# Optimization experiments

Hardware: AMD Instinct MI355X
Metric: run time of the kernel (lower is better)

## Reference

```python
import jax, jax.numpy as jnp
import numpy as np

PMASK_SLOPE = 5.0
SAMPLE_SLOPE = 10.0
SPARSITY = 0.125
MAX_ITERS = 1000
ATOL = 1e-3

B, H, W = 64, 256, 256


def _rejection_sample(x, key):
    """Regenerate uniform noise until mean(x > prob) ~= mean(x), like
    ThresholdRandomMaskSigmoidV1.forward. Returns (result, prob)."""
    tgt = jnp.mean(x)

    def draw(k):
        k, sub = jax.random.split(k)
        prob = jax.random.uniform(sub, x.shape, x.dtype)
        result = (x > prob).astype(x.dtype)
        return k, prob, result

    def cond(state):
        _, _, result, count = state
        ok = jnp.isclose(jnp.mean(result), tgt, atol=ATOL)
        return jnp.logical_and(jnp.logical_not(ok), count <= MAX_ITERS)

    def body(state):
        k, _, _, count = state
        k, prob, result = draw(k)
        return (k, prob, result, count + 1)

    k, prob0, result0 = draw(key)
    _, prob, result, _ = jax.lax.while_loop(cond, body, (k, prob0, result0, jnp.int32(0)))
    return result, prob


def _make_threshold(key):
    @jax.custom_vjp
    def thresh(x):
        return _rejection_sample(x, key)[0]

    def fwd(x):
        result, prob = _rejection_sample(x, key)
        return result, (x, prob)

    def bwd(res, g):
        x, prob = res
        e = jnp.exp(-SAMPLE_SLOPE * (x - prob))
        return (SAMPLE_SLOPE * e / (e + 1.0) ** 2 * g,)

    thresh.defvjp(fwd, bwd)
    return thresh

_thresh = _make_threshold(jax.random.key(42))


def setup_inputs() -> dict:
    key = jax.random.key(0)
    kx, kw = jax.random.split(key)
    x = jax.random.normal(kx, (B, 1, H, W), dtype=jnp.float32)
    eps = 1e-4
    u = jax.random.uniform(kw, (1, 1, H, W), dtype=jnp.float32, minval=eps, maxval=1.0 - eps)
    weight = -jnp.log(1.0 / u - 1.0) / PMASK_SLOPE  # ProbMask.reset_parameters
    return {"x": x, "weight": weight}


def reference(x, weight):
    # ProbMask: broadcast weight against x[..., 0:1] then sigmoid(slope * .)
    prob1 = jax.nn.sigmoid(PMASK_SLOPE * (0.0 * x[..., 0:1] + weight))  # [B,1,H,W]

    # RescaleProbMap
    xbar = jnp.mean(prob1)
    r = SPARSITY / xbar
    beta = (1.0 - SPARSITY) / (1.0 - xbar)
    le = (r < 1.0).astype(prob1.dtype)
    prob2 = le * prob1 * r + (1.0 - le) * (1.0 - (1.0 - prob1) * beta)

    # ThresholdRandomMaskSigmoidV1 (rejection-sampled binary mask)
    mask = _thresh(prob2)  # [B,1,H,W]

    # FFT: torch.rfft(x, 2, onesided=False) -> full 2D FFT of real input
    fc = jnp.fft.fft2(x[:, 0])                       # [B,H,W] complex
    fft = jnp.stack([fc.real, fc.imag], axis=1)      # [B,2,H,W]

    # UnderSample: multiply both channels by the mask
    u_k = fft * mask                                  # broadcast [B,1,H,W]

    # iFFT over spatial dims
    uc = u_k[:, 0] + 1j * u_k[:, 1]
    ic = jnp.fft.ifft2(uc)
    uifft = jnp.stack([ic.real, ic.imag], axis=1)    # [B,2,H,W]

    # ComplexAbs
    complex_abs = jnp.sqrt(uifft[:, 0:1] ** 2 + uifft[:, 1:2] ** 2)

    return (uifft, complex_abs, mask, fft, u_k)
```

## Files before the change

kernel.cpp:

```cpp
#include <hip/hip_runtime.h>


#define HW_N   65536

__device__ __forceinline__ float f_add(float a, float b){ float d; asm("v_add_f32 %0, %1, %2" : "=v"(d) : "v"(a), "v"(b)); return d; }
__device__ __forceinline__ float f_sub(float a, float b){ float d; asm("v_sub_f32 %0, %1, %2" : "=v"(d) : "v"(a), "v"(b)); return d; }
__device__ __forceinline__ float f_mul(float a, float b){ float d; asm("v_mul_f32 %0, %1, %2" : "=v"(d) : "v"(a), "v"(b)); return d; }
__device__ __forceinline__ float f_fma(float a, float b, float c){ return __builtin_fmaf(a, b, c); }

__device__ float xla_expf(float x0) {
  float x = fminf(x0, 88.723f);
  float m = floorf(f_fma(x, 1.44269504088896341f, 0.5f));
  float r = f_fma(m, -0.693359375f, x);
  r = f_fma(m, 2.12194440e-4f, r);
  float r2 = f_mul(r, r);
  float r3 = f_mul(r2, r);
  float y  = f_fma(1.9875691500E-4f, r, 1.3981999507E-3f);
  float y1 = f_fma(4.1665795894E-2f, r, 1.6666665459E-1f);
  float y2 = f_add(r, 1.0f);
  y  = f_fma(y, r, 8.3334519073E-3f);
  y1 = f_fma(y1, r, 5.0000001201E-1f);
  y  = f_fma(y, r3, y1);
  y  = f_fma(y, r2, y2);
  float p2n = __uint_as_float((unsigned)(((int)m + 127) << 23));
  float res = f_mul(y, p2n);
  if (x0 < -104.0f) res = 0.0f;
  return fmaxf(res, x0);
}

__device__ __forceinline__ float xla_sigmoid(float q) {
  float e = xla_expf(-q);
  return 1.0f / f_add(1.0f, e);
}

__host__ __device__ __forceinline__ void tf2x32(unsigned k0, unsigned k1,
                                                unsigned c0, unsigned c1,
                                                unsigned& o0, unsigned& o1) {
  unsigned ks2 = k0 ^ k1 ^ 0x1BD11BDAu;
  unsigned x0 = c0 + k0, x1 = c1 + k1;
#define TF_R(r) { x0 += x1; x1 = (x1 << r) | (x1 >> (32 - r)); x1 ^= x0; }
  TF_R(13) TF_R(15) TF_R(26) TF_R(6)
  x0 += k1;  x1 += ks2 + 1u;
  TF_R(17) TF_R(29) TF_R(16) TF_R(24)
  x0 += ks2; x1 += k0 + 2u;
  TF_R(13) TF_R(15) TF_R(26) TF_R(6)
  x0 += k0;  x1 += k1 + 3u;
  TF_R(17) TF_R(29) TF_R(16) TF_R(24)
  x0 += k1;  x1 += ks2 + 4u;
  TF_R(13) TF_R(15) TF_R(26) TF_R(6)
  x0 += ks2; x1 += k0 + 5u;
#undef TF_R
  o0 = x0; o1 = x1;
}

__global__ void k_prep(const float* __restrict__ weight, float* __restrict__ ws) {
  int i = blockIdx.x * 256 + threadIdx.x;
  if (i < HW_N) {
    float q = f_mul(5.0f, weight[i]);
    ws[i] = xla_sigmoid(q);
  }
  if (blockIdx.x == 0 && threadIdx.x < 128) {
    double ang = -2.0 * 3.14159265358979323846 * (double)threadIdx.x / 256.0;
    float* tw = ws + 2 * HW_N;
    tw[2 * threadIdx.x]     = (float)cos(ang);
    tw[2 * threadIdx.x + 1] = (float)sin(ang);
  }
}

__global__ void k_xbar(float* __restrict__ ws) {
  __shared__ float lanes[32];
  int l = threadIdx.x;
  if (l < 32) {
    float acc = 0.0f;
    for (int k = 0; k < 2048; ++k)
      acc = f_add(acc, ws[32 * k + l]);
    lanes[l] = acc;
  }
  __syncthreads();
  if (l == 0) {
    float A[32];
    for (int i = 0; i < 32; ++i) A[i] = lanes[i];
    float c[16];
    for (int k = 0; k < 16; ++k) c[k] = f_add(A[k], A[k + 16]);
    float d[8];
    for (int k = 0; k < 8; ++k)  d[k] = f_add(c[k], c[k + 8]);
    float e[4];
    for (int k = 0; k < 4; ++k)  e[k] = f_add(d[k], d[k + 4]);
    float f2[2];
    for (int k = 0; k < 2; ++k)  f2[k] = f_add(e[k], e[k + 2]);
    float S = f_add(f2[0], f2[1]);
    float xbar = S / 65536.0f;
    float r    = 0.125f / xbar;
    float le   = (r < 1.0f) ? 1.0f : 0.0f;
    float beta = 0.875f / f_sub(1.0f, xbar);
    float* sc = ws + 2 * HW_N + 256;
    sc[0] = r; sc[1] = le; sc[2] = beta;
  }
}

__global__ void k_prob2(float* __restrict__ ws) {
  int i = blockIdx.x * 256 + threadIdx.x;
  if (i >= HW_N) return;
  const float* sc = ws + 2 * HW_N + 256;
  float r = sc[0], le = sc[1], beta = sc[2];
  float p = ws[i];
  float t1 = f_mul(f_mul(le, p), r);
  float t2 = f_mul(f_sub(1.0f, le),
                   f_sub(1.0f, f_mul(f_sub(1.0f, p), beta)));
  ws[HW_N + i] = f_add(t1, t2);
}

__global__ void k_mask(const float* __restrict__ ws, float* __restrict__ mask,
                       unsigned sk0, unsigned sk1) {
  unsigned i = blockIdx.x * 256u + threadIdx.x;
  unsigned o0, o1;
  tf2x32(sk0, sk1, 0u, i, o0, o1);
  unsigned bits = o0 ^ o1;
  float f = __uint_as_float((bits >> 9) | 0x3f800000u) - 1.0f;
  float p2 = ws[HW_N + (i & 65535u)];
  mask[i] = (p2 > f) ? 1.0f : 0.0f;
}

__device__ __forceinline__ int brev8(int i) { return (int)(__brev((unsigned)i) >> 24); }

__device__ __forceinline__ void fft256(float* re, float* im, int k,
                                       const float* __restrict__ tw, float sgn) {
  for (int s = 1; s <= 8; ++s) {
    __syncthreads();
    int hm = 1 << (s - 1);
    int j  = k & (hm - 1);
    int i1 = ((k >> (s - 1)) << s) + j;
    int i2 = i1 + hm;
    int ti = j << (8 - s);
    float wr = tw[2 * ti], wi = sgn * tw[2 * ti + 1];
    float vr = re[i2], vi = im[i2];
    float tr  = vr * wr - vi * wi;
    float tii = vr * wi + vi * wr;
    float ur = re[i1], ui = im[i1];
    re[i1] = ur + tr;  im[i1] = ui + tii;
    re[i2] = ur - tr;  im[i2] = ui - tii;
  }
  __syncthreads();
}

__global__ void k_fft_row(const float* __restrict__ x, float* __restrict__ fft,
                          const float* __restrict__ ws) {
  __shared__ float re[2][256], im[2][256];
  const float* tw = ws + 2 * HW_N;
  int line = blockIdx.x * 2 + (threadIdx.x >> 7);
  int k = threadIdx.x & 127, r = threadIdx.x >> 7;
  int b = line >> 8, h = line & 255;
  const float* src = x + b * 65536 + h * 256;
  re[r][k]       = src[brev8(k)];        im[r][k]       = 0.0f;
  re[r][k + 128] = src[brev8(k + 128)];  im[r][k + 128] = 0.0f;
  fft256(re[r], im[r], k, tw, 1.0f);
  float* dre = fft + b * 131072 + h * 256;
  float* dim = dre + 65536;
  dre[k]       = re[r][k];        dim[k]       = im[r][k];
  dre[k + 128] = re[r][k + 128];  dim[k + 128] = im[r][k + 128];
}

__global__ __launch_bounds__(256) void k_colpass(float* __restrict__ fftbuf,
                                                 const float* __restrict__ mask,
                                                 float* __restrict__ uk,
                                                 float* __restrict__ vbuf,
                                                 const float* __restrict__ ws) {
  __shared__ float lre[256][32];
  __shared__ float lim[256][32];
  const float* tw = ws + 2 * HW_N;
  int bid = blockIdx.x;
  int b = bid >> 3, c0 = (bid & 7) << 5;
  int t = threadIdx.x;
  int cl = t & 31, rg = t >> 5;
  float* pre = fftbuf + b * 131072;
  float* pim = pre + 65536;

  for (int it = 0; it < 32; ++it) {
    int r = (it << 3) + rg;
    int cc = (cl + r) & 31;
    lre[r][cc] = pre[r * 256 + c0 + cl];
    lim[r][cc] = pim[r * 256 + c0 + cl];
  }
  __syncthreads();

  for (int hm = 128, sh = 7; hm >= 1; hm >>= 1, --sh) {
    for (int kk = 0; kk < 16; ++kk) {
      int k = (kk << 3) + rg;
      int j = k & (hm - 1);
      int i1 = ((k >> sh) << (sh + 1)) + j;
      int i2 = i1 + hm;
      int ti = j << (7 - sh);
      float wr = tw[2 * ti], wi = tw[2 * ti + 1];
      int cc1 = (cl + i1) & 31, cc2 = (cl + i2) & 31;
      float ur = lre[i1][cc1], ui = lim[i1][cc1];
      float vr = lre[i2][cc2], vi = lim[i2][cc2];
      float dr = ur - vr, di = ui - vi;
      lre[i1][cc1] = ur + vr;            lim[i1][cc1] = ui + vi;
      lre[i2][cc2] = dr * wr - di * wi;  lim[i2][cc2] = dr * wi + di * wr;
    }
    __syncthreads();
  }

  const float* mk = mask + b * 65536;
  float* ukre = uk + b * 131072;
  float* ukim = ukre + 65536;
  for (int it = 0; it < 32; ++it) {
    int p = (it << 3) + rg;
    int f = brev8(p);
    int cc = (cl + p) & 31;
    float vr = lre[p][cc], vi = lim[p][cc];
    int gi = f * 256 + c0 + cl;
    pre[gi] = vr;  pim[gi] = vi;
    float m = mk[gi];
    float mvr = vr * m, mvi = vi * m;
    ukre[gi] = mvr;  ukim[gi] = mvi;
    lre[p][cc] = mvr;  lim[p][cc] = mvi;
  }
  __syncthreads();

  for (int s = 1; s <= 8; ++s) {
    int hm = 1 << (s - 1);
    for (int kk = 0; kk < 16; ++kk) {
      int k = (kk << 3) + rg;
      int j = k & (hm - 1);
      int i1 = ((k >> (s - 1)) << s) + j;
      int i2 = i1 + hm;
      int ti = j << (8 - s);
      float wr = tw[2 * ti], wi = -tw[2 * ti + 1];
      int cc1 = (cl + i1) & 31, cc2 = (cl + i2) & 31;
      float vr = lre[i2][cc2], vi = lim[i2][cc2];
      float tr = vr * wr - vi * wi, tii = vr * wi + vi * wr;
      float ur = lre[i1][cc1], ui = lim[i1][cc1];
      lre[i1][cc1] = ur + tr;  lim[i1][cc1] = ui + tii;
      lre[i2][cc2] = ur - tr;  lim[i2][cc2] = ui - tii;
    }
    __syncthreads();
  }

  float* vre = vbuf + b * 131072;
  float* vim = vre + 65536;
  for (int it = 0; it < 32; ++it) {
    int r = (it << 3) + rg;
    int cc = (cl + r) & 31;
    vre[r * 256 + c0 + cl] = lre[r][cc];
    vim[r * 256 + c0 + cl] = lim[r][cc];
  }
}

__global__ void k_irow(float* __restrict__ uif, float* __restrict__ cabs,
                       const float* __restrict__ ws) {
  __shared__ float re[2][256], im[2][256];
  const float* tw = ws + 2 * HW_N;
  int line = blockIdx.x * 2 + (threadIdx.x >> 7);
  int k = threadIdx.x & 127, r = threadIdx.x >> 7;
  int b = line >> 8, h = line & 255;
  float* sre = uif + b * 131072 + h * 256;
  float* sim = sre + 65536;
  re[r][k]       = sre[brev8(k)];        im[r][k]       = sim[brev8(k)];
  re[r][k + 128] = sre[brev8(k + 128)];  im[r][k + 128] = sim[brev8(k + 128)];
  fft256(re[r], im[r], k, tw, -1.0f);
  const float scale = 1.0f / 65536.0f;
  float* ab = cabs + b * 65536 + h * 256;
  for (int t2 = 0; t2 < 2; ++t2) {
    int i = k + t2 * 128;
    float vr = re[r][i] * scale, vi = im[r][i] * scale;
    sre[i] = vr;  sim[i] = vi;
    ab[i] = sqrtf(vr * vr + vi * vi);
  }
}

extern "C" void kernel_launch(void* const* d_in, const int* in_sizes, int n_in,
                              void* d_out, int out_size, void* d_ws, size_t ws_size,
                              hipStream_t stream) {
  const float* x      = (const float*)d_in[0];
  const float* weight = (const float*)d_in[1];
  float* out = (float*)d_out;
  float* ws  = (float*)d_ws;

  float* uifft = out;
  float* cabs  = out + 8388608;
  float* mask  = out + 12582912;
  float* fft   = out + 16777216;
  float* uk    = out + 25165824;

  unsigned sk0, sk1;
  tf2x32(0u, 42u, 0u, 1u, sk0, sk1);

  k_prep   <<<256, 256, 0, stream>>>(weight, ws);
  k_xbar   <<<1, 64, 0, stream>>>(ws);
  k_prob2  <<<256, 256, 0, stream>>>(ws);
  k_mask   <<<16384, 256, 0, stream>>>(ws, mask, sk0, sk1);
  k_fft_row<<<8192, 256, 0, stream>>>(x, fft, ws);
  k_colpass<<<512, 256, 0, stream>>>(fft, mask, uk, uifft, ws);
  k_irow   <<<8192, 256, 0, stream>>>(uifft, cabs, ws);
}
```

Baseline: 279.3 us.

## Switch row and column FFTs to radix-4 and fuse prob2 into mask

Replaces the radix-2 FFTs (8 stages) in the row, column and inverse-row kernels with radix-4 butterflies (4 stages). This halves the shared-memory passes and barriers, and the row kernels now process 4 lines per block with padded LDS to avoid bank conflicts. Twiddle tables grow to 256 entries for the 3*ti indices, and bit reversal becomes base-4 digit reversal. The prob2 rescale is folded into the mask kernel, removing one launch and a global round trip. Floating-point rounding may differ slightly from the radix-2 ordering.

New measurement: 274.5 us. About the same (-1.7%).

```diff
diff --git a/kernel.cpp b/kernel.cpp
--- a/kernel.cpp
+++ b/kernel.cpp
@@ -1,7 +1,8 @@
 #include <hip/hip_runtime.h>
 
 
-#define HW_N   65536
+#define HW_N 65536
+#define LMAP(a) ((a) + ((a) >> 5))
 
 __device__ __forceinline__ float f_add(float a, float b){ float d; asm("v_add_f32 %0, %1, %2" : "=v"(d) : "v"(a), "v"(b)); return d; }
 __device__ __forceinline__ float f_sub(float a, float b){ float d; asm("v_sub_f32 %0, %1, %2" : "=v"(d) : "v"(a), "v"(b)); return d; }
@@ -27,7 +28,6 @@
   if (x0 < -104.0f) res = 0.0f;
   return fmaxf(res, x0);
 }
-
 __device__ __forceinline__ float xla_sigmoid(float q) {
   float e = xla_expf(-q);
   return 1.0f / f_add(1.0f, e);
@@ -53,17 +53,27 @@
   o0 = x0; o1 = x1;
 }
 
+__device__ __forceinline__ int rev4(int p) {
+  return ((p & 3) << 6) | (((p >> 2) & 3) << 4) | (((p >> 4) & 3) << 2) | ((p >> 6) & 3);
+}
+
+#define CMULW(xr, xi, ti) { float wr = tw[2*(ti)], wi = tw[2*(ti)+1]; \
+  float nr = xr*wr - xi*wi; xi = xr*wi + xi*wr; xr = nr; }
+#define CMULWC(xr, xi, ti) { float wr = tw[2*(ti)], wi = tw[2*(ti)+1]; \
+  float nr = xr*wr + xi*wi; xi = xi*wr - xr*wi; xr = nr; }
+
 __global__ void k_prep(const float* __restrict__ weight, float* __restrict__ ws) {
   int i = blockIdx.x * 256 + threadIdx.x;
   if (i < HW_N) {
     float q = f_mul(5.0f, weight[i]);
     ws[i] = xla_sigmoid(q);
   }
-  if (blockIdx.x == 0 && threadIdx.x < 128) {
-    double ang = -2.0 * 3.14159265358979323846 * (double)threadIdx.x / 256.0;
-    float* tw = ws + 2 * HW_N;
-    tw[2 * threadIdx.x]     = (float)cos(ang);
-    tw[2 * threadIdx.x + 1] = (float)sin(ang);
+  if (blockIdx.x == 0) {
+    int t = threadIdx.x;
+    double ang = -2.0 * 3.14159265358979323846 * (double)t / 256.0;
+    float* tw = ws + 131072;
+    tw[2 * t]     = (float)cos(ang);
+    tw[2 * t + 1] = (float)sin(ang);
   }
 }
 
@@ -93,71 +103,77 @@
     float r    = 0.125f / xbar;
     float le   = (r < 1.0f) ? 1.0f : 0.0f;
     float beta = 0.875f / f_sub(1.0f, xbar);
-    float* sc = ws + 2 * HW_N + 256;
+    float* sc = ws + 131584;
     sc[0] = r; sc[1] = le; sc[2] = beta;
   }
-}
-
-__global__ void k_prob2(float* __restrict__ ws) {
-  int i = blockIdx.x * 256 + threadIdx.x;
-  if (i >= HW_N) return;
-  const float* sc = ws + 2 * HW_N + 256;
-  float r = sc[0], le = sc[1], beta = sc[2];
-  float p = ws[i];
-  float t1 = f_mul(f_mul(le, p), r);
-  float t2 = f_mul(f_sub(1.0f, le),
-                   f_sub(1.0f, f_mul(f_sub(1.0f, p), beta)));
-  ws[HW_N + i] = f_add(t1, t2);
 }
 
 __global__ void k_mask(const float* __restrict__ ws, float* __restrict__ mask,
                        unsigned sk0, unsigned sk1) {
   unsigned i = blockIdx.x * 256u + threadIdx.x;
+  const float* sc = ws + 131584;
+  float r = sc[0], le = sc[1], beta = sc[2];
+  float p1 = ws[i & 65535u];
+  float t1 = f_mul(f_mul(le, p1), r);
+  float t2 = f_mul(f_sub(1.0f, le),
+                   f_sub(1.0f, f_mul(f_sub(1.0f, p1), beta)));
+  float p2 = f_add(t1, t2);
   unsigned o0, o1;
   tf2x32(sk0, sk1, 0u, i, o0, o1);
   unsigned bits = o0 ^ o1;
   float f = __uint_as_float((bits >> 9) | 0x3f800000u) - 1.0f;
-  float p2 = ws[HW_N + (i & 65535u)];
   mask[i] = (p2 > f) ? 1.0f : 0.0f;
 }
 
-__device__ __forceinline__ int brev8(int i) { return (int)(__brev((unsigned)i) >> 24); }
-
-__device__ __forceinline__ void fft256(float* re, float* im, int k,
-                                       const float* __restrict__ tw, float sgn) {
-  for (int s = 1; s <= 8; ++s) {
-    __syncthreads();
-    int hm = 1 << (s - 1);
-    int j  = k & (hm - 1);
-    int i1 = ((k >> (s - 1)) << s) + j;
-    int i2 = i1 + hm;
-    int ti = j << (8 - s);
-    float wr = tw[2 * ti], wi = sgn * tw[2 * ti + 1];
-    float vr = re[i2], vi = im[i2];
-    float tr  = vr * wr - vi * wi;
-    float tii = vr * wi + vi * wr;
-    float ur = re[i1], ui = im[i1];
-    re[i1] = ur + tr;  im[i1] = ui + tii;
-    re[i2] = ur - tr;  im[i2] = ui - tii;
-  }
-  __syncthreads();
-}
-
-__global__ void k_fft_row(const float* __restrict__ x, float* __restrict__ fft,
-                          const float* __restrict__ ws) {
-  __shared__ float re[2][256], im[2][256];
-  const float* tw = ws + 2 * HW_N;
-  int line = blockIdx.x * 2 + (threadIdx.x >> 7);
-  int k = threadIdx.x & 127, r = threadIdx.x >> 7;
+__global__ __launch_bounds__(256) void k_fft_row(const float* __restrict__ x,
+                                                 float* __restrict__ fftb,
+                                                 const float* __restrict__ ws) {
+  __shared__ float re[4][264], im[4][264];
+  const float* tw = ws + 131072;
+  int rl = threadIdx.x >> 6, bf = threadIdx.x & 63;
+  int line = blockIdx.x * 4 + rl;
   int b = line >> 8, h = line & 255;
   const float* src = x + b * 65536 + h * 256;
-  re[r][k]       = src[brev8(k)];        im[r][k]       = 0.0f;
-  re[r][k + 128] = src[brev8(k + 128)];  im[r][k + 128] = 0.0f;
-  fft256(re[r], im[r], k, tw, 1.0f);
-  float* dre = fft + b * 131072 + h * 256;
+  float* lre = re[rl];
+  float* lim = im[rl];
+  #pragma unroll
+  for (int t2 = 0; t2 < 4; ++t2) {
+    int p = t2 * 64 + bf;
+    lre[LMAP(p)] = src[rev4(p)];
+    lim[LMAP(p)] = 0.0f;
+  }
+  #pragma unroll
+  for (int s2 = 0; s2 < 4; ++s2) {
+    __syncthreads();
+    int lq = 2 * s2, qq = 1 << lq;
+    int j = bf & (qq - 1), g = bf >> lq;
+    int base = (g << (lq + 2)) + j;
+    int u = 64 >> lq;
+    int a0 = base, a1 = base + qq, a2 = base + 2 * qq, a3 = base + 3 * qq;
+    float s0r = lre[LMAP(a0)], s0i = lim[LMAP(a0)];
+    float s1r = lre[LMAP(a1)], s1i = lim[LMAP(a1)];
+    float s2r = lre[LMAP(a2)], s2i = lim[LMAP(a2)];
+    float s3r = lre[LMAP(a3)], s3i = lim[LMAP(a3)];
+    int ti = j * u;
+    CMULW(s1r, s1i, ti); CMULW(s2r, s2i, 2 * ti); CMULW(s3r, s3i, 3 * ti);
+    float p0r = s0r + s2r, p0i = s0i + s2i;
+    float m0r = s0r - s2r, m0i = s0i - s2i;
+    float p1r = s1r + s3r, p1i = s1i + s3i;
+    float m1r = s1r - s3r, m1i = s1i - s3i;
+    lre[LMAP(a0)] = p0r + p1r;  lim[LMAP(a0)] = p0i + p1i;
+    lre[LMAP(a1)] = m0r + m1i;  lim[LMAP(a1)] = m0i - m1r;
+    lre[LMAP(a2)] = p0r - p1r;  lim[LMAP(a2)] = p0i - p1i;
+    lre[LMAP(a3)] = m0r - m1i;  lim[LMAP(a3)] = m0i + m1r;
+  }
+  __syncthreads();
+  float* dre = fftb + b * 131072 + h * 256;
   float* dim = dre + 65536;
-  dre[k]       = re[r][k];        dim[k]       = im[r][k];
-  dre[k + 128] = re[r][k + 128];  dim[k + 128] = im[r][k + 128];
+  #pragma unroll
+  for (int t2 = 0; t2 < 4; ++t2) {
+    int p = t2 * 64 + bf;
+    dre[p] = lre[LMAP(p)];
+    dim[p] = lim[LMAP(p)];
+  }
 }
 
 __global__ __launch_bounds__(256) void k_colpass(float* __restrict__ fftbuf,
@@ -167,7 +183,7 @@
                                                  const float* __restrict__ ws) {
   __shared__ float lre[256][32];
   __shared__ float lim[256][32];
-  const float* tw = ws + 2 * HW_N;
+  const float* tw = ws + 131072;
   int bid = blockIdx.x;
   int b = bid >> 3, c0 = (bid & 7) << 5;
   int t = threadIdx.x;
@@ -181,32 +197,46 @@
     lre[r][cc] = pre[r * 256 + c0 + cl];
     lim[r][cc] = pim[r * 256 + c0 + cl];
   }
-  __syncthreads();
-
-  for (int hm = 128, sh = 7; hm >= 1; hm >>= 1, --sh) {
-    for (int kk = 0; kk < 16; ++kk) {
-      int k = (kk << 3) + rg;
-      int j = k & (hm - 1);
-      int i1 = ((k >> sh) << (sh + 1)) + j;
-      int i2 = i1 + hm;
-      int ti = j << (7 - sh);
-      float wr = tw[2 * ti], wi = tw[2 * ti + 1];
-      int cc1 = (cl + i1) & 31, cc2 = (cl + i2) & 31;
-      float ur = lre[i1][cc1], ui = lim[i1][cc1];
-      float vr = lre[i2][cc2], vi = lim[i2][cc2];
-      float dr = ur - vr, di = ui - vi;
-      lre[i1][cc1] = ur + vr;            lim[i1][cc1] = ui + vi;
-      lre[i2][cc2] = dr * wr - di * wi;  lim[i2][cc2] = dr * wi + di * wr;
+
+  #pragma unroll
+  for (int s2 = 0; s2 < 4; ++s2) {
+    __syncthreads();
+    int lq = 6 - 2 * s2, qq = 1 << lq;
+    int u = 1 << (2 * s2);
+    for (int kk = 0; kk < 8; ++kk) {
+      int bf = (kk << 3) + rg;
+      int j = bf & (qq - 1), g = bf >> lq;
+      int base = (g << (lq + 2)) + j;
+      int a0 = base, a1 = base + qq, a2 = base + 2 * qq, a3 = base + 3 * qq;
+      int c_0 = (cl + a0) & 31, c_1 = (cl + a1) & 31,
+          c_2 = (cl + a2) & 31, c_3 = (cl + a3) & 31;
+      float ar = lre[a0][c_0], ai = lim[a0][c_0];
+      float br = lre[a1][c_1], bi = lim[a1][c_1];
+      float cr = lre[a2][c_2], ci = lim[a2][c_2];
+      float dr = lre[a3][c_3], di = lim[a3][c_3];
+      float apcr = ar + cr, apci = ai + ci;
+      float amcr = ar - cr, amci = ai - ci;
+      float bpdr = br + dr, bpdi = bi + di;
+      float bmdr = br - dr, bmdi = bi - di;
+      int ti = j * u;
+      float y1r = amcr + bmdi, y1i = amci - bmdr;
+      float y2r = apcr - bpdr, y2i = apci - bpdi;
+      float y3r = amcr - bmdi, y3i = amci + bmdr;
+      CMULW(y1r, y1i, ti); CMULW(y2r, y2i, 2 * ti); CMULW(y3r, y3i, 3 * ti);
+      lre[a0][c_0] = apcr + bpdr;  lim[a0][c_0] = apci + bpdi;
+      lre[a1][c_1] = y1r;          lim[a1][c_1] = y1i;
+      lre[a2][c_2] = y2r;          lim[a2][c_2] = y2i;
+      lre[a3][c_3] = y3r;          lim[a3][c_3] = y3i;
     }
-    __syncthreads();
-  }
+  }
+  __syncthreads();
 
   const float* mk = mask + b * 65536;
   float* ukre = uk + b * 131072;
   float* ukim = ukre + 65536;
   for (int it = 0; it < 32; ++it) {
     int p = (it << 3) + rg;
-    int f = brev8(p);
+    int f = rev4(p);
     int cc = (cl + p) & 31;
     float vr = lre[p][cc], vi = lim[p][cc];
     int gi = f * 256 + c0 + cl;
@@ -216,26 +246,36 @@
     ukre[gi] = mvr;  ukim[gi] = mvi;
     lre[p][cc] = mvr;  lim[p][cc] = mvi;
   }
-  __syncthreads();
-
-  for (int s = 1; s <= 8; ++s) {
-    int hm = 1 << (s - 1);
-    for (int kk = 0; kk < 16; ++kk) {
-      int k = (kk << 3) + rg;
-      int j = k & (hm - 1);
-      int i1 = ((k >> (s - 1)) << s) + j;
-      int i2 = i1 + hm;
-      int ti = j << (8 - s);
-      float wr = tw[2 * ti], wi = -tw[2 * ti + 1];
-      int cc1 = (cl + i1) & 31, cc2 = (cl + i2) & 31;
-      float vr = lre[i2][cc2], vi = lim[i2][cc2];
-      float tr = vr * wr - vi * wi, tii = vr * wi + vi * wr;
-      float ur = lre[i1][cc1], ui = lim[i1][cc1];
-      lre[i1][cc1] = ur + tr;  lim[i1][cc1] = ui + tii;
-      lre[i2][cc2] = ur - tr;  lim[i2][cc2] = ui - tii;
+
+  #pragma unroll
+  for (int s2 = 0; s2 < 4; ++s2) {
+    __syncthreads();
+    int lq = 2 * s2, qq = 1 << lq;
+    int u = 64 >> lq;
+    for (int kk = 0; kk < 8; ++kk) {
+      int bf = (kk << 3) + rg;
+      int j = bf & (qq - 1), g = bf >> lq;
+      int base = (g << (lq + 2)) + j;
+      int a0 = base, a1 = base + qq, a2 = base + 2 * qq, a3 = base + 3 * qq;
+      int c_0 = (cl + a0) & 31, c_1 = (cl + a1) & 31,
+          c_2 = (cl + a2) & 31, c_3 = (cl + a3) & 31;
+      float s0r = lre[a0][c_0], s0i = lim[a0][c_0];
+      float s1r = lre[a1][c_1], s1i = lim[a1][c_1];
+      float s2r = lre[a2][c_2], s2i = lim[a2][c_2];
+      float s3r = lre[a3][c_3], s3i = lim[a3][c_3];
+      int ti = j * u;
+      CMULWC(s1r, s1i, ti); CMULWC(s2r, s2i, 2 * ti); CMULWC(s3r, s3i, 3 * ti);
+      float p0r = s0r + s2r, p0i = s0i + s2i;
+      float m0r = s0r - s2r, m0i = s0i - s2i;
+      float p1r = s1r + s3r, p1i = s1i + s3i;
+      float m1r = s1r - s3r, m1i = s1i - s3i;
+      lre[a0][c_0] = p0r + p1r;  lim[a0][c_0] = p0i + p1i;
+      lre[a1][c_1] = m0r - m1i;  lim[a1][c_1] = m0i + m1r;
+      lre[a2][c_2] = p0r - p1r;  lim[a2][c_2] = p0i - p1i;
+      lre[a3][c_3] = m0r + m1i;  lim[a3][c_3] = m0i - m1r;
     }
-    __syncthreads();
-  }
+  }
+  __syncthreads();
 
   float* vre = vbuf + b * 131072;
   float* vim = vre + 65536;
@@ -247,25 +287,57 @@
   }
 }
 
-__global__ void k_irow(float* __restrict__ uif, float* __restrict__ cabs,
-                       const float* __restrict__ ws) {
-  __shared__ float re[2][256], im[2][256];
-  const float* tw = ws + 2 * HW_N;
-  int line = blockIdx.x * 2 + (threadIdx.x >> 7);
-  int k = threadIdx.x & 127, r = threadIdx.x >> 7;
+__global__ __launch_bounds__(256) void k_irow(float* __restrict__ uif,
+                                              float* __restrict__ cabs,
+                                              const float* __restrict__ ws) {
+  __shared__ float re[4][264], im[4][264];
+  const float* tw = ws + 131072;
+  int rl = threadIdx.x >> 6, bf = threadIdx.x & 63;
+  int line = blockIdx.x * 4 + rl;
   int b = line >> 8, h = line & 255;
   float* sre = uif + b * 131072 + h * 256;
   float* sim = sre + 65536;
-  re[r][k]       = sre[brev8(k)];        im[r][k]       = sim[brev8(k)];
-  re[r][k + 128] = sre[brev8(k + 128)];  im[r][k + 128] = sim[brev8(k + 128)];
-  fft256(re[r], im[r], k, tw, -1.0f);
+  float* lre = re[rl];
+  float* lim = im[rl];
+  #pragma unroll
+  for (int t2 = 0; t2 < 4; ++t2) {
+    int p = t2 * 64 + bf;
+    int q = rev4(p);
+    lre[LMAP(p)] = sre[q];
+    lim[LMAP(p)] = sim[q];
+  }
+  #pragma unroll
+  for (int s2 = 0; s2 < 4; ++s2) {
+    __syncthreads();
+    int lq = 2 * s2, qq = 1 << lq;
+    int j = bf & (qq - 1), g = bf >> lq;
+    int base = (g << (lq + 2)) + j;
+    int u = 64 >> lq;
+    int a0 = base, a1 = base + qq, a2 = base + 2 * qq, a3 = base + 3 * qq;
+    float s0r = lre[LMAP(a0)], s0i = lim[LMAP(a0)];
+    float s1r = lre[LMAP(a1)], s1i = lim[LMAP(a1)];
+    float s2r = lre[LMAP(a2)], s2i = lim[LMAP(a2)];
+    float s3r = lre[LMAP(a3)], s3i = lim[LMAP(a3)];
+    int ti = j * u;
+    CMULWC(s1r, s1i, ti); CMULWC(s2r, s2i, 2 * ti); CMULWC(s3r, s3i, 3 * ti);
+    float p0r = s0r + s2r, p0i = s0i + s2i;
+    float m0r = s0r - s2r, m0i = s0i - s2i;
+    float p1r = s1r + s3r, p1i = s1i + s3i;
+    float m1r = s1r - s3r, m1i = s1i - s3i;
+    lre[LMAP(a0)] = p0r + p1r;  lim[LMAP(a0)] = p0i + p1i;
+    lre[LMAP(a1)] = m0r - m1i;  lim[LMAP(a1)] = m0i + m1r;
+    lre[LMAP(a2)] = p0r - p1r;  lim[LMAP(a2)] = p0i - p1i;
+    lre[LMAP(a3)] = m0r + m1i;  lim[LMAP(a3)] = m0i - m1r;
+  }
+  __syncthreads();
   const float scale = 1.0f / 65536.0f;
   float* ab = cabs + b * 65536 + h * 256;
-  for (int t2 = 0; t2 < 2; ++t2) {
-    int i = k + t2 * 128;
-    float vr = re[r][i] * scale, vi = im[r][i] * scale;
-    sre[i] = vr;  sim[i] = vi;
-    ab[i] = sqrtf(vr * vr + vi * vi);
+  #pragma unroll
+  for (int t2 = 0; t2 < 4; ++t2) {
+    int p = t2 * 64 + bf;
+    float vr = lre[LMAP(p)] * scale, vi = lim[LMAP(p)] * scale;
+    sre[p] = vr;  sim[p] = vi;
+    ab[p] = sqrtf(vr * vr + vi * vi);
   }
 }
 
@@ -288,9 +360,8 @@
 
   k_prep   <<<256, 256, 0, stream>>>(weight, ws);
   k_xbar   <<<1, 64, 0, stream>>>(ws);
-  k_prob2  <<<256, 256, 0, stream>>>(ws);
   k_mask   <<<16384, 256, 0, stream>>>(ws, mask, sk0, sk1);
-  k_fft_row<<<8192, 256, 0, stream>>>(x, fft, ws);
+  k_fft_row<<<4096, 256, 0, stream>>>(x, fft, ws);
   k_colpass<<<512, 256, 0, stream>>>(fft, mask, uk, uifft, ws);
-  k_irow   <<<8192, 256, 0, stream>>>(uifft, cabs, ws);
-}
+  k_irow   <<<4096, 256, 0, stream>>>(uifft, cabs, ws);
+}
```
